# Kernel optimization log

Measured on AMD Instinct MI355X. Metric: run time of the kernel, lower is better.

Reference implementation:

```python
import jax, jax.numpy as jnp
import numpy as np
from jax import lax

M, B, L, Q, S = 4, 64, 512, 512, 26  # models, batch, seq_len, hmm states, alphabet


def setup_inputs() -> dict:
    key = jax.random.key(0)
    k1, k2, k3, k4 = jax.random.split(key, 4)
    inputs = jax.random.uniform(k1, (M, B, L, S), dtype=jnp.float32)
    A_logits = jax.random.normal(k2, (M, Q, Q), dtype=jnp.float32)
    init_logits = jax.random.normal(k3, (M, Q), dtype=jnp.float32)
    em_logits = jax.random.normal(k4, (M, Q, S), dtype=jnp.float32)
    return {"inputs": inputs, "A_logits": A_logits,
            "init_logits": init_logits, "em_logits": em_logits}


def reference(inputs, A_logits, init_logits, em_logits):
    """Profile-HMM forward algorithm (scaled), as run by the MsaHmmCell RNN.

    inputs:      [M, B, L, S] observation probabilities (one-hot or soft)
    A_logits:    [M, Q, Q]    transition logits (row-softmax -> stochastic A)
    init_logits: [M, Q]       initial state distribution logits
    em_logits:   [M, Q, S]    emission logits (softmax over alphabet)
    returns loglik [M, B]  (the tensor the layer returns)
    """
    A = jax.nn.softmax(A_logits, axis=-1)        # [M, Q, Q]
    pi = jax.nn.softmax(init_logits, axis=-1)    # [M, Q]
    Bem = jax.nn.softmax(em_logits, axis=-1)     # [M, Q, S]

    # per-step emission likelihoods, time-major for scan: [L, M, B, Q]
    E = jnp.einsum('mbls,mqs->lmbq', inputs, Bem)

    # t = 0: alpha_0 = pi * e_0, scaled
    a0 = pi[:, None, :] * E[0]                   # [M, B, Q]
    s0 = jnp.sum(a0, axis=-1, keepdims=True)
    carry0 = (a0 / s0, jnp.log(s0[..., 0]))      # (alpha [M,B,Q], loglik [M,B])

    def step(carry, e_t):
        alpha, ll = carry
        r = jnp.einsum('mbq,mqp->mbp', alpha, A)  # transition
        a = r * e_t                               # emission
        s = jnp.sum(a, axis=-1, keepdims=True)    # scaling factor
        return (a / s, ll + jnp.log(s[..., 0])), None

    (alpha, loglik), _ = lax.scan(step, carry0, E[1:])
    return loglik  # [M, B] == reshape(loglik, (num_models, -1)) in the layer
```

## Files before the change

kernel.cpp:

```cpp
#include <hip/hip_runtime.h>
#include <hip/hip_bf16.h>
#include <math.h>


#define MM 4
#define BB 64
#define LL 512
#define QQ 512
#define SS 26
#define ASTR 528

typedef float f32x4 __attribute__((ext_vector_type(4)));
typedef int i32x4 __attribute__((ext_vector_type(4)));
typedef int i32x8 __attribute__((ext_vector_type(8)));

__device__ __forceinline__ float bf2f(unsigned short u) {
    return __uint_as_float(((unsigned)u) << 16);
}
__device__ __forceinline__ unsigned short f2bf(float f) {
    unsigned u = __float_as_uint(f);
    u = u + 0x7FFFu + ((u >> 16) & 1u);
    return (unsigned short)(u >> 16);
}
__device__ __forceinline__ unsigned char f2fp8(float x) {
    int r = __builtin_amdgcn_cvt_pk_fp8_f32(x, x, 0, false);
    return (unsigned char)(r & 0xFF);
}
__device__ __forceinline__ i32x8 ld32B(const unsigned char* p) {
    i32x4 lo = *(const i32x4*)p;
    i32x4 hi = *(const i32x4*)(p + 16);
    return __builtin_shufflevector(lo, hi, 0, 1, 2, 3, 4, 5, 6, 7);
}
#define MFMA8(A, B, C) __builtin_amdgcn_mfma_scale_f32_16x16x128_f8f6f4( \
    (A), (B), (C), 0, 0, 0, 0x7F7F7F7F, 0, 0x7F7F7F7F)
#define SGB __builtin_amdgcn_sched_group_barrier
__device__ __forceinline__ void barrier_lds() {
    __asm__ __volatile__("" ::: "memory");
    __builtin_amdgcn_s_waitcnt(0xC07F);
    __builtin_amdgcn_s_barrier();
    __asm__ __volatile__("" ::: "memory");
}


__global__ void prep_small(const float* __restrict__ il, const float* __restrict__ em,
                           float* __restrict__ pi, float* __restrict__ Bem) {
    int blk = blockIdx.x;
    int m = blk / (QQ + 1);
    int r = blk % (QQ + 1);
    int lane = threadIdx.x;
    if (r < QQ) {
        float x = (lane < SS) ? em[((size_t)m * QQ + r) * SS + lane] : -1e30f;
        float mx = x;
        #pragma unroll
        for (int o = 1; o < 64; o <<= 1) mx = fmaxf(mx, __shfl_xor(mx, o));
        float e = (lane < SS) ? __expf(x - mx) : 0.f;
        float s = e;
        #pragma unroll
        for (int o = 1; o < 64; o <<= 1) s += __shfl_xor(s, o);
        if (lane < SS) Bem[((size_t)m * QQ + r) * SS + lane] = e / s;
    } else {
        float v[8];
        float mx = -1e30f;
        #pragma unroll
        for (int k = 0; k < 8; ++k) { v[k] = il[m * QQ + k * 64 + lane]; mx = fmaxf(mx, v[k]); }
        #pragma unroll
        for (int o = 1; o < 64; o <<= 1) mx = fmaxf(mx, __shfl_xor(mx, o));
        float s = 0.f;
        #pragma unroll
        for (int k = 0; k < 8; ++k) { v[k] = __expf(v[k] - mx); s += v[k]; }
        #pragma unroll
        for (int o = 1; o < 64; o <<= 1) s += __shfl_xor(s, o);
        #pragma unroll
        for (int k = 0; k < 8; ++k) pi[m * QQ + k * 64 + lane] = v[k] / s;
    }
}

__global__ void prep_arow(const float* __restrict__ Al, float* __restrict__ Lrow) {
    int row = blockIdx.x;
    int lane = threadIdx.x;
    const float* p = Al + (size_t)row * QQ;
    float v[8];
    float mx = -1e30f;
    #pragma unroll
    for (int k = 0; k < 8; ++k) { v[k] = p[k * 64 + lane]; mx = fmaxf(mx, v[k]); }
    #pragma unroll
    for (int o = 1; o < 64; o <<= 1) mx = fmaxf(mx, __shfl_xor(mx, o));
    float s = 0.f;
    #pragma unroll
    for (int k = 0; k < 8; ++k) s += __expf(v[k] - mx);
    #pragma unroll
    for (int o = 1; o < 64; o <<= 1) s += __shfl_xor(s, o);
    if (lane == 0) Lrow[row] = mx + __logf(s);
}

__global__ void prep_atq(const float* __restrict__ Al, const float* __restrict__ Lrow,
                         unsigned char* __restrict__ Atq) {
    int bid = blockIdx.x;
    int m = bid >> 3, pb = bid & 7;
    __shared__ unsigned char tile[64][68];
    int l6 = threadIdx.x & 63, g = threadIdx.x >> 6;
    for (int c = 0; c < 8; ++c) {
        #pragma unroll
        for (int r = 0; r < 16; ++r) {
            int ql = g * 16 + r;
            int q = c * 64 + ql;
            float x = Al[((size_t)m * QQ + q) * QQ + pb * 64 + l6];
            tile[ql][l6] = f2fp8(__expf(x - Lrow[m * QQ + q]) * 256.f);
        }
        __syncthreads();
        #pragma unroll
        for (int r = 0; r < 16; ++r) {
            int pr = g * 16 + r;
            Atq[((size_t)m * QQ + pb * 64 + pr) * QQ + c * 64 + l6] = tile[l6][pr];
        }
        __syncthreads();
    }
}

__global__ void prep_e(const float* __restrict__ inp, const float* __restrict__ Bem,
                       unsigned short* __restrict__ E) {
    int bid = blockIdx.x;
    int tc = bid & 7;
    int b = (bid >> 3) & 63;
    int m = bid >> 9;
    int q0 = threadIdx.x;
    float bem0[SS], bem1[SS];
    const float* bp = Bem + (size_t)m * QQ * SS;
    #pragma unroll
    for (int j = 0; j < SS; ++j) bem0[j] = bp[(size_t)q0 * SS + j];
    #pragma unroll
    for (int j = 0; j < SS; ++j) bem1[j] = bp[(size_t)(q0 + 256) * SS + j];
    const float* ip = inp + (((size_t)(m * BB + b)) * LL + tc * 64) * SS;
    for (int lt = 0; lt < 64; ++lt) {
        int t = tc * 64 + lt;
        float a0 = 0.f, a1 = 0.f;
        #pragma unroll
        for (int j = 0; j < SS; ++j) {
            float x = ip[lt * SS + j];
            a0 += x * bem0[j];
            a1 += x * bem1[j];
        }
        size_t o = (((size_t)m * LL + t) * BB + b) * QQ + q0;
        E[o] = f2bf(a0);
        E[o + 256] = f2bf(a1);
    }
}


__launch_bounds__(512, 2)
__global__ void hmm_scan(const unsigned short* __restrict__ E,
                         const unsigned char* __restrict__ Atq,
                         const float* __restrict__ pi,
                         float* __restrict__ out) {
    const int c = blockIdx.x;
    const int m = c >> 2, bg = c & 3;
    const int tid = threadIdx.x;
    const int lane = tid & 63;
    const int wv = tid >> 6;
    const int sl = lane & 15;
    const int quad = lane >> 4;
    const float LOG256 = 5.545177444479562f;

    __shared__ unsigned char albuf[2][16 * ASTR];
    __shared__ __align__(16) float psl[2][16][36];
    __shared__ float Sfin[2][16];

    i32x8 breg[4][4];
    {
        const unsigned char* Ab = Atq + (size_t)m * QQ * QQ;
        #pragma unroll
        for (int h = 0; h < 4; ++h) {
            int p = wv * 64 + h * 16 + sl;
            const unsigned char* rp = Ab + (size_t)p * QQ + quad * 32;
            #pragma unroll
            for (int kc = 0; kc < 4; ++kc)
                breg[h][kc] = ld32B(rp + kc * 128);
        }
    }

    int wq[4];
    #pragma unroll
    for (int h = 0; h < 4; ++h)
        wq[h] = sl * ASTR + wv * 64 + h * 16 + quad * 4;

    const int b = bg * 16 + sl;
    const size_t ebase = (size_t)m * LL * BB * QQ;
    const ushort4* __restrict__ E4 = (const ushort4*)(E + ebase);
    const unsigned ESTR4 = (BB * QQ) >> 2;
    const unsigned ebq = (unsigned)(b * QQ) >> 2;
    unsigned eoffs[4];
    #pragma unroll
    for (int h = 0; h < 4; ++h) eoffs[h] = (unsigned)(wv * 16 + h * 4 + quad);

    float v[4][4];
    ushort4 ea[4], eb[4];

    float gcur, gprev, ll;
    const int pslot = 4 * wv + quad;

    {
        #pragma unroll
        for (int h = 0; h < 4; ++h) ea[h] = E4[ebq + ESTR4 + eoffs[h]];
        #pragma unroll
        for (int h = 0; h < 4; ++h) {
            int p0 = wv * 64 + h * 16 + quad * 4;
            f32x4 pv = *(const f32x4*)(pi + m * QQ + p0);
            ushort4 e0 = E4[ebq + eoffs[h]];
            v[h][0] = pv[0] * bf2f(e0.x);
            v[h][1] = pv[1] * bf2f(e0.y);
            v[h][2] = pv[2] * bf2f(e0.z);
            v[h][3] = pv[3] * bf2f(e0.w);
        }
        gcur = 256.f;
        gprev = 1.0f;
        unsigned char* ab = &albuf[0][0];
        #pragma unroll
        for (int h = 0; h < 4; ++h) {
            int d = __builtin_amdgcn_cvt_pk_fp8_f32(gcur * v[h][0], gcur * v[h][1], 0, false);
            d = __builtin_amdgcn_cvt_pk_fp8_f32(gcur * v[h][2], gcur * v[h][3], d, true);
            *(int*)(ab + wq[h]) = d;
        }
        float ps = ((v[0][0] + v[0][1]) + (v[0][2] + v[0][3]))
                 + ((v[1][0] + v[1][1]) + (v[1][2] + v[1][3]))
                 + ((v[2][0] + v[2][1]) + (v[2][2] + v[2][3]))
                 + ((v[3][0] + v[3][1]) + (v[3][2] + v[3][3]));
        psl[0][sl][pslot] = ps;
        ll = -(__logf(gcur) + LOG256);
        barrier_lds();
    }

    auto body = [&](int par, bool first, ushort4 (&ecur)[4], ushort4 (&enxt)[4],
                    unsigned epre) {
        #pragma unroll
        for (int h = 0; h < 4; ++h) enxt[h] = E4[epre + eoffs[h]];

        if (wv == 0 && lane < 16) {
            const f32x4* pr = (const f32x4*)&psl[par][lane][0];
            f32x4 s0 = (pr[0] + pr[1]) + (pr[2] + pr[3]);
            f32x4 s1 = (pr[4] + pr[5]) + (pr[6] + pr[7]);
            f32x4 ss4 = s0 + s1;
            Sfin[par][lane] = (ss4[0] + ss4[1]) + (ss4[2] + ss4[3]);
        }
        float lam = first ? 16384.0f
                          : 16384.0f * gcur * gprev * Sfin[par ^ 1][sl];
        float gnext = 128.0f * __builtin_amdgcn_rcpf(lam);

        const unsigned char* ar = &albuf[par][0] + sl * ASTR + quad * 32;

        f32x4 a0 = (f32x4){0.f, 0.f, 0.f, 0.f};
        f32x4 a1 = a0, a2 = a0, a3 = a0;
        i32x8 af0 = ld32B(ar);
        a0 = MFMA8(breg[0][0], af0, a0);
        a1 = MFMA8(breg[1][0], af0, a1);
        a2 = MFMA8(breg[2][0], af0, a2);
        a3 = MFMA8(breg[3][0], af0, a3);
        i32x8 af1 = ld32B(ar + 128);
        a0 = MFMA8(breg[0][1], af1, a0);
        a1 = MFMA8(breg[1][1], af1, a1);
        a2 = MFMA8(breg[2][1], af1, a2);
        a3 = MFMA8(breg[3][1], af1, a3);
        i32x8 af2 = ld32B(ar + 256);
        a0 = MFMA8(breg[0][2], af2, a0);
        a1 = MFMA8(breg[1][2], af2, a1);
        a2 = MFMA8(breg[2][2], af2, a2);
        a3 = MFMA8(breg[3][2], af2, a3);
        i32x8 af3 = ld32B(ar + 384);
        a0 = MFMA8(breg[0][3], af3, a0);
        a1 = MFMA8(breg[1][3], af3, a1);
        a2 = MFMA8(breg[2][3], af3, a2);
        a3 = MFMA8(breg[3][3], af3, a3);
        SGB(0x100, 1, 0);
        SGB(0x100, 2, 0); SGB(0x8, 4, 0);
        SGB(0x100, 2, 0); SGB(0x8, 4, 0);
        SGB(0x100, 2, 0); SGB(0x8, 4, 0);
        SGB(0x100, 2, 0); SGB(0x8, 4, 0);

        unsigned char* ab = &albuf[par ^ 1][0];
        v[0][0] = a0[0] * bf2f(ecur[0].x);
        v[0][1] = a0[1] * bf2f(ecur[0].y);
        v[0][2] = a0[2] * bf2f(ecur[0].z);
        v[0][3] = a0[3] * bf2f(ecur[0].w);
        v[1][0] = a1[0] * bf2f(ecur[1].x);
        v[1][1] = a1[1] * bf2f(ecur[1].y);
        v[1][2] = a1[2] * bf2f(ecur[1].z);
        v[1][3] = a1[3] * bf2f(ecur[1].w);
        v[2][0] = a2[0] * bf2f(ecur[2].x);
        v[2][1] = a2[1] * bf2f(ecur[2].y);
        v[2][2] = a2[2] * bf2f(ecur[2].z);
        v[2][3] = a2[3] * bf2f(ecur[2].w);
        v[3][0] = a3[0] * bf2f(ecur[3].x);
        v[3][1] = a3[1] * bf2f(ecur[3].y);
        v[3][2] = a3[2] * bf2f(ecur[3].z);
        v[3][3] = a3[3] * bf2f(ecur[3].w);
        #pragma unroll
        for (int h = 0; h < 4; ++h) {
            int d = __builtin_amdgcn_cvt_pk_fp8_f32(gnext * v[h][0], gnext * v[h][1], 0, false);
            d = __builtin_amdgcn_cvt_pk_fp8_f32(gnext * v[h][2], gnext * v[h][3], d, true);
            *(int*)(ab + wq[h]) = d;
        }
        float ps = ((v[0][0] + v[0][1]) + (v[0][2] + v[0][3]))
                 + ((v[1][0] + v[1][1]) + (v[1][2] + v[1][3]))
                 + ((v[2][0] + v[2][1]) + (v[2][2] + v[2][3]))
                 + ((v[3][0] + v[3][1]) + (v[3][2] + v[3][3]));
        psl[par ^ 1][sl][pslot] = ps;
        ll -= __logf(gnext) + LOG256;
        gprev = gcur; gcur = gnext;
        barrier_lds();
    };

    unsigned epre = ebq + 2 * ESTR4;
    body(0, true,  ea, eb, epre); epre += ESTR4;
    body(1, false, eb, ea, epre); epre += ESTR4;
    for (int t = 2; t < LL - 2; t += 2) {
        body(0, false, ea, eb, epre); epre += ESTR4;
        body(1, false, eb, ea, epre); epre += ESTR4;
    }
    {
        const unsigned char* ar = &albuf[0][0] + sl * ASTR + quad * 32;
        i32x8 af0 = ld32B(ar);
        i32x8 af1 = ld32B(ar + 128);
        i32x8 af2 = ld32B(ar + 256);
        i32x8 af3 = ld32B(ar + 384);
        f32x4 a0 = (f32x4){0.f, 0.f, 0.f, 0.f};
        f32x4 a1 = a0, a2 = a0, a3 = a0;
        a0 = MFMA8(breg[0][0], af0, a0);  a1 = MFMA8(breg[1][0], af0, a1);
        a2 = MFMA8(breg[2][0], af0, a2);  a3 = MFMA8(breg[3][0], af0, a3);
        a0 = MFMA8(breg[0][1], af1, a0);  a1 = MFMA8(breg[1][1], af1, a1);
        a2 = MFMA8(breg[2][1], af1, a2);  a3 = MFMA8(breg[3][1], af1, a3);
        a0 = MFMA8(breg[0][2], af2, a0);  a1 = MFMA8(breg[1][2], af2, a1);
        a2 = MFMA8(breg[2][2], af2, a2);  a3 = MFMA8(breg[3][2], af2, a3);
        a0 = MFMA8(breg[0][3], af3, a0);  a1 = MFMA8(breg[1][3], af3, a1);
        a2 = MFMA8(breg[2][3], af3, a2);  a3 = MFMA8(breg[3][3], af3, a3);
        v[0][0] = a0[0] * bf2f(ea[0].x);
        v[0][1] = a0[1] * bf2f(ea[0].y);
        v[0][2] = a0[2] * bf2f(ea[0].z);
        v[0][3] = a0[3] * bf2f(ea[0].w);
        v[1][0] = a1[0] * bf2f(ea[1].x);
        v[1][1] = a1[1] * bf2f(ea[1].y);
        v[1][2] = a1[2] * bf2f(ea[1].z);
        v[1][3] = a1[3] * bf2f(ea[1].w);
        v[2][0] = a2[0] * bf2f(ea[2].x);
        v[2][1] = a2[1] * bf2f(ea[2].y);
        v[2][2] = a2[2] * bf2f(ea[2].z);
        v[2][3] = a2[3] * bf2f(ea[2].w);
        v[3][0] = a3[0] * bf2f(ea[3].x);
        v[3][1] = a3[1] * bf2f(ea[3].y);
        v[3][2] = a3[2] * bf2f(ea[3].z);
        v[3][3] = a3[3] * bf2f(ea[3].w);
    }

    {
        float ps = ((v[0][0] + v[0][1]) + (v[0][2] + v[0][3]))
                 + ((v[1][0] + v[1][1]) + (v[1][2] + v[1][3]))
                 + ((v[2][0] + v[2][1]) + (v[2][2] + v[2][3]))
                 + ((v[3][0] + v[3][1]) + (v[3][2] + v[3][3]));
        psl[1][sl][pslot] = ps;
        __syncthreads();
        if (wv == 0 && lane < 16) {
            const f32x4* pr = (const f32x4*)&psl[1][lane][0];
            f32x4 s0 = (pr[0] + pr[1]) + (pr[2] + pr[3]);
            f32x4 s1 = (pr[4] + pr[5]) + (pr[6] + pr[7]);
            f32x4 ss4 = s0 + s1;
            float S = (ss4[0] + ss4[1]) + (ss4[2] + ss4[3]);
            out[m * BB + bg * 16 + lane] = ll + __logf(S);
        }
    }
}


extern "C" void kernel_launch(void* const* d_in, const int* in_sizes, int n_in,
                              void* d_out, int out_size, void* d_ws, size_t ws_size,
                              hipStream_t stream) {
    const float* inputs = (const float*)d_in[0];
    const float* A_logits = (const float*)d_in[1];
    const float* init_logits = (const float*)d_in[2];
    const float* em_logits = (const float*)d_in[3];
    float* out = (float*)d_out;

    char* ws = (char*)d_ws;
    size_t off = 0;
    unsigned short* E = (unsigned short*)(ws + off);  off += (size_t)MM * LL * BB * QQ * 2;
    unsigned char* Atq = (unsigned char*)(ws + off);  off += (size_t)MM * QQ * QQ;
    float* Bem = (float*)(ws + off);                  off += (size_t)MM * QQ * SS * 4;
    float* pi = (float*)(ws + off);                   off += (size_t)MM * QQ * 4;
    float* Lrow = (float*)(ws + off);                 off += (size_t)MM * QQ * 4;

    if (ws_size < off) {
        (void)hipMemsetAsync(d_out, 0, (size_t)out_size * sizeof(float), stream);
        return;
    }

    prep_small<<<dim3(MM * (QQ + 1)), dim3(64), 0, stream>>>(init_logits, em_logits, pi, Bem);
    prep_arow<<<dim3(MM * QQ), dim3(64), 0, stream>>>(A_logits, Lrow);
    prep_atq<<<dim3(MM * 8), dim3(256), 0, stream>>>(A_logits, Lrow, Atq);
    prep_e<<<dim3(MM * BB * 8), dim3(256), 0, stream>>>(inputs, Bem, E);
    hmm_scan<<<dim3(16), dim3(512), 0, stream>>>(E, Atq, pi, out);
}
```

Before: 626.2 us.

## Re-layout alpha LDS buffer into 16-byte chunks and pre-reduce partial sums via shuffle

```diff
diff --git a/kernel.cpp b/kernel.cpp
--- a/kernel.cpp
+++ b/kernel.cpp
@@ -8,7 +8,6 @@
 #define LL 512
 #define QQ 512
 #define SS 26
-#define ASTR 528
 
 typedef float f32x4 __attribute__((ext_vector_type(4)));
 typedef int i32x4 __attribute__((ext_vector_type(4)));
@@ -26,6 +25,11 @@
     int r = __builtin_amdgcn_cvt_pk_fp8_f32(x, x, 0, false);
     return (unsigned char)(r & 0xFF);
 }
+__device__ __forceinline__ i32x8 ld2t(const unsigned char* p) {
+    i32x4 lo = *(const i32x4*)p;
+    i32x4 hi = *(const i32x4*)(p + 256);
+    return __builtin_shufflevector(lo, hi, 0, 1, 2, 3, 4, 5, 6, 7);
+}
 __device__ __forceinline__ i32x8 ld32B(const unsigned char* p) {
     i32x4 lo = *(const i32x4*)p;
     i32x4 hi = *(const i32x4*)(p + 16);
@@ -33,7 +37,6 @@
 }
 #define MFMA8(A, B, C) __builtin_amdgcn_mfma_scale_f32_16x16x128_f8f6f4( \
     (A), (B), (C), 0, 0, 0, 0x7F7F7F7F, 0, 0x7F7F7F7F)
-#define SGB __builtin_amdgcn_sched_group_barrier
 __device__ __forceinline__ void barrier_lds() {
     __asm__ __volatile__("" ::: "memory");
     __builtin_amdgcn_s_waitcnt(0xC07F);
@@ -161,8 +164,8 @@
     const int quad = lane >> 4;
     const float LOG256 = 5.545177444479562f;
 
-    __shared__ unsigned char albuf[2][16 * ASTR];
-    __shared__ __align__(16) float psl[2][16][36];
+    __shared__ unsigned char albuf[2][32][16][16];
+    __shared__ __align__(16) float psl[2][16][20];
     __shared__ float Sfin[2][16];
 
     i32x8 breg[4][4];
@@ -181,7 +184,8 @@
     int wq[4];
     #pragma unroll
     for (int h = 0; h < 4; ++h)
-        wq[h] = sl * ASTR + wv * 64 + h * 16 + quad * 4;
+        wq[h] = (wv * 4 + h) * 256 + sl * 16 + quad * 4;
+    const int rq = quad * 512 + sl * 16;
 
     const int b = bg * 16 + sl;
     const size_t ebase = (size_t)m * LL * BB * QQ;
@@ -196,7 +200,6 @@
     ushort4 ea[4], eb[4];
 
     float gcur, gprev, ll;
-    const int pslot = 4 * wv + quad;
 
     {
         #pragma unroll
@@ -213,7 +216,7 @@
         }
         gcur = 256.f;
         gprev = 1.0f;
-        unsigned char* ab = &albuf[0][0];
+        unsigned char* ab = &albuf[0][0][0][0];
         #pragma unroll
         for (int h = 0; h < 4; ++h) {
             int d = __builtin_amdgcn_cvt_pk_fp8_f32(gcur * v[h][0], gcur * v[h][1], 0, false);
@@ -224,7 +227,8 @@
                  + ((v[1][0] + v[1][1]) + (v[1][2] + v[1][3]))
                  + ((v[2][0] + v[2][1]) + (v[2][2] + v[2][3]))
                  + ((v[3][0] + v[3][1]) + (v[3][2] + v[3][3]));
-        psl[0][sl][pslot] = ps;
+        ps += __shfl_xor(ps, 16);
+        if ((quad & 1) == 0) psl[0][sl][2 * wv + (quad >> 1)] = ps;
         ll = -(__logf(gcur) + LOG256);
         barrier_lds();
     }
@@ -236,46 +240,39 @@
 
         if (wv == 0 && lane < 16) {
             const f32x4* pr = (const f32x4*)&psl[par][lane][0];
-            f32x4 s0 = (pr[0] + pr[1]) + (pr[2] + pr[3]);
-            f32x4 s1 = (pr[4] + pr[5]) + (pr[6] + pr[7]);
-            f32x4 ss4 = s0 + s1;
+            f32x4 ss4 = (pr[0] + pr[1]) + (pr[2] + pr[3]);
             Sfin[par][lane] = (ss4[0] + ss4[1]) + (ss4[2] + ss4[3]);
         }
         float lam = first ? 16384.0f
                           : 16384.0f * gcur * gprev * Sfin[par ^ 1][sl];
         float gnext = 128.0f * __builtin_amdgcn_rcpf(lam);
 
-        const unsigned char* ar = &albuf[par][0] + sl * ASTR + quad * 32;
+        const unsigned char* ar = &albuf[par][0][0][0] + rq;
+        i32x8 af0 = ld2t(ar);
+        i32x8 af1 = ld2t(ar + 2048);
+        i32x8 af2 = ld2t(ar + 4096);
+        i32x8 af3 = ld2t(ar + 6144);
 
         f32x4 a0 = (f32x4){0.f, 0.f, 0.f, 0.f};
         f32x4 a1 = a0, a2 = a0, a3 = a0;
-        i32x8 af0 = ld32B(ar);
         a0 = MFMA8(breg[0][0], af0, a0);
         a1 = MFMA8(breg[1][0], af0, a1);
         a2 = MFMA8(breg[2][0], af0, a2);
         a3 = MFMA8(breg[3][0], af0, a3);
-        i32x8 af1 = ld32B(ar + 128);
         a0 = MFMA8(breg[0][1], af1, a0);
         a1 = MFMA8(breg[1][1], af1, a1);
         a2 = MFMA8(breg[2][1], af1, a2);
         a3 = MFMA8(breg[3][1], af1, a3);
-        i32x8 af2 = ld32B(ar + 256);
         a0 = MFMA8(breg[0][2], af2, a0);
         a1 = MFMA8(breg[1][2], af2, a1);
         a2 = MFMA8(breg[2][2], af2, a2);
         a3 = MFMA8(breg[3][2], af2, a3);
-        i32x8 af3 = ld32B(ar + 384);
         a0 = MFMA8(breg[0][3], af3, a0);
         a1 = MFMA8(breg[1][3], af3, a1);
         a2 = MFMA8(breg[2][3], af3, a2);
         a3 = MFMA8(breg[3][3], af3, a3);
-        SGB(0x100, 1, 0);
-        SGB(0x100, 2, 0); SGB(0x8, 4, 0);
-        SGB(0x100, 2, 0); SGB(0x8, 4, 0);
-        SGB(0x100, 2, 0); SGB(0x8, 4, 0);
-        SGB(0x100, 2, 0); SGB(0x8, 4, 0);
-
-        unsigned char* ab = &albuf[par ^ 1][0];
+
+        unsigned char* ab = &albuf[par ^ 1][0][0][0];
         v[0][0] = a0[0] * bf2f(ecur[0].x);
         v[0][1] = a0[1] * bf2f(ecur[0].y);
         v[0][2] = a0[2] * bf2f(ecur[0].z);
@@ -302,7 +299,8 @@
                  + ((v[1][0] + v[1][1]) + (v[1][2] + v[1][3]))
                  + ((v[2][0] + v[2][1]) + (v[2][2] + v[2][3]))
                  + ((v[3][0] + v[3][1]) + (v[3][2] + v[3][3]));
-        psl[par ^ 1][sl][pslot] = ps;
+        ps += __shfl_xor(ps, 16);
+        if ((quad & 1) == 0) psl[par ^ 1][sl][2 * wv + (quad >> 1)] = ps;
         ll -= __logf(gnext) + LOG256;
         gprev = gcur; gcur = gnext;
         barrier_lds();
@@ -316,11 +314,11 @@
         body(1, false, eb, ea, epre); epre += ESTR4;
     }
     {
-        const unsigned char* ar = &albuf[0][0] + sl * ASTR + quad * 32;
-        i32x8 af0 = ld32B(ar);
-        i32x8 af1 = ld32B(ar + 128);
-        i32x8 af2 = ld32B(ar + 256);
-        i32x8 af3 = ld32B(ar + 384);
+        const unsigned char* ar = &albuf[0][0][0][0] + rq;
+        i32x8 af0 = ld2t(ar);
+        i32x8 af1 = ld2t(ar + 2048);
+        i32x8 af2 = ld2t(ar + 4096);
+        i32x8 af3 = ld2t(ar + 6144);
         f32x4 a0 = (f32x4){0.f, 0.f, 0.f, 0.f};
         f32x4 a1 = a0, a2 = a0, a3 = a0;
         a0 = MFMA8(breg[0][0], af0, a0);  a1 = MFMA8(breg[1][0], af0, a1);
@@ -354,13 +352,12 @@
                  + ((v[1][0] + v[1][1]) + (v[1][2] + v[1][3]))
                  + ((v[2][0] + v[2][1]) + (v[2][2] + v[2][3]))
                  + ((v[3][0] + v[3][1]) + (v[3][2] + v[3][3]));
-        psl[1][sl][pslot] = ps;
+        ps += __shfl_xor(ps, 16);
+        if ((quad & 1) == 0) psl[1][sl][2 * wv + (quad >> 1)] = ps;
         __syncthreads();
         if (wv == 0 && lane < 16) {
             const f32x4* pr = (const f32x4*)&psl[1][lane][0];
-            f32x4 s0 = (pr[0] + pr[1]) + (pr[2] + pr[3]);
-            f32x4 s1 = (pr[4] + pr[5]) + (pr[6] + pr[7]);
-            f32x4 ss4 = s0 + s1;
+            f32x4 ss4 = (pr[0] + pr[1]) + (pr[2] + pr[3]);
             float S = (ss4[0] + ss4[1]) + (ss4[2] + ss4[3]);
             out[m * BB + bg * 16 + lane] = ll + __logf(S);
         }
```

After: 629.1 us. About the same (+0.5%).
